# Kernel tuning notes

Hardware: AMD Instinct MI355X
Metric: run time of the kernel (lower is better)

## Reference

```python
import jax, jax.numpy as jnp
import numpy as np

B = 2048      # number of scenes (samples)
A = 64        # max agents per scene
D = 128       # latent_size (embed dim)
H = 4         # heads (hardcoded in module)
HD = D // H   # head dim = 32
NEG = -1e9


def setup_inputs() -> dict:
    key = jax.random.key(0)
    k1, k2, k3, k4 = jax.random.split(key, 4)
    # flat ragged agent features; only the first sum(agents) rows are 'real'
    att_in = jax.random.normal(k1, (B * A, D), dtype=jnp.float32)
    agents_per_sample = jax.random.randint(k2, (B,), 1, A + 1)  # each scene has >=1 agent
    s = 1.0 / np.sqrt(D)
    w_in = jax.random.uniform(k3, (3 * D, D), minval=-s, maxval=s, dtype=jnp.float32)
    b_in = jnp.zeros((3 * D,), dtype=jnp.float32)
    w_out = jax.random.uniform(k4, (D, D), minval=-s, maxval=s, dtype=jnp.float32)
    b_out = jnp.zeros((D,), dtype=jnp.float32)
    return {"att_in": att_in, "w_in": w_in, "b_in": b_in,
            "w_out": w_out, "b_out": b_out, "agents_per_sample": agents_per_sample}


def reference(att_in, w_in, b_in, w_out, b_out, agents_per_sample):
    # scatter flat ragged rows into padded [B, A, D] (same as padded_att_in[mask] = att_in)
    offsets = jnp.cumsum(agents_per_sample) - agents_per_sample          # exclusive prefix sum
    idx = offsets[:, None] + jnp.arange(A)[None, :]                      # [B, A] flat row index
    mask = jnp.arange(A)[None, :] < agents_per_sample[:, None]          # [B, A] valid-agent mask
    padded = jnp.take(att_in, idx, axis=0) * mask[..., None].astype(att_in.dtype)
    # fused in-projection (nn.MultiheadAttention in_proj)
    qkv = padded @ w_in.T + b_in                                        # [B, A, 3D]
    q, k, v = jnp.split(qkv, 3, axis=-1)
    q = q.reshape(B, A, H, HD)
    k = k.reshape(B, A, H, HD)
    v = v.reshape(B, A, H, HD)
    scores = jnp.einsum('bqhd,bkhd->bhqk', q, k) / np.sqrt(HD).astype(q.dtype)
    # key_padding_mask: padded keys excluded from softmax
    scores = jnp.where(mask[:, None, None, :], scores, NEG)
    attn = jax.nn.softmax(scores, axis=-1)
    ctx = jnp.einsum('bhqk,bkhd->bqhd', attn, v).reshape(B, A, D)
    out = (ctx @ w_out.T + b_out) * mask[..., None].astype(ctx.dtype)   # zero out padded rows (torch slices them off)
    return out
```

## Files before the change

### kernel.cpp

```cpp
#include <hip/hip_runtime.h>
#include <hip/hip_bf16.h>

typedef __bf16 bf16;
typedef __bf16 bf16x4 __attribute__((ext_vector_type(4)));
typedef __bf16 bf16x8 __attribute__((ext_vector_type(8)));
typedef float  f32x4  __attribute__((ext_vector_type(4)));

#define NEG_INF (-1e9f)
#define N_SCENES 2048

__global__ __launch_bounds__(256) void prep_kernel(
    const float* __restrict__ w_in, const float* __restrict__ w_out,
    const int* __restrict__ agents,
    bf16* __restrict__ w_in_b, bf16* __restrict__ w_out_b, int* __restrict__ offs)
{
    __shared__ int tot[256];
    const int t = threadIdx.x;
    if (blockIdx.x == 0) {
        int loc[8]; int s = 0;
        #pragma unroll
        for (int j = 0; j < 8; ++j) { loc[j] = agents[t * 8 + j]; s += loc[j]; }
        tot[t] = s;
        __syncthreads();
        for (int o = 1; o < 256; o <<= 1) {
            int v = (t >= o) ? tot[t - o] : 0;
            __syncthreads();
            tot[t] += v;
            __syncthreads();
        }
        int run = tot[t] - s;
        #pragma unroll
        for (int j = 0; j < 8; ++j) { offs[t * 8 + j] = run; run += loc[j]; }
    } else {
        int i = (blockIdx.x - 1) * 1024 + t * 4;
        float4 v; bf16* dst;
        if (i < 49152) { v = *(const float4*)(w_in + i);            dst = w_in_b + i; }
        else           { v = *(const float4*)(w_out + (i - 49152)); dst = w_out_b + (i - 49152); }
        bf16x4 o = { (bf16)v.x, (bf16)v.y, (bf16)v.z, (bf16)v.w };
        *(bf16x4*)dst = o;
    }
}

__global__ __launch_bounds__(256, 3) void attn_kernel(
    const float* __restrict__ att_in,
    const float* __restrict__ b_in, const float* __restrict__ b_out,
    const bf16* __restrict__ w_in_b, const bf16* __restrict__ w_out_b,
    const int* __restrict__ agents, const int* __restrict__ offs,
    float* __restrict__ out)
{
    __shared__ bf16 s_lds[4 * 6144];

    const int b    = blockIdx.x;
    const int tid  = threadIdx.x;
    const int lane = tid & 63;
    const int w    = tid >> 6;
    const int h    = w;
    const int r    = lane & 15;
    const int qd   = lane >> 4;
    const int q1   = qd & 1;
    const int qh   = qd >> 1;
    const int nb   = agents[b];
    const int off  = offs[b];
    const int mtc  = (nb + 15) >> 4;

    bf16* Qld = s_lds + w * 6144;
    bf16* Kld = Qld + 2048;
    bf16* vT  = Qld + 4096;

    {
        const float4 z4 = make_float4(0.f, 0.f, 0.f, 0.f);
        const int nz = (64 - nb) * 32;
        for (int i = tid; i < nz; i += 256) {
            int row = nb + (i >> 5);
            *(float4*)(out + ((size_t)b * 64 + row) * 128 + (i & 31) * 4) = z4;
        }
    }

    {
        bf16x4 z4 = {(bf16)0.f,(bf16)0.f,(bf16)0.f,(bf16)0.f};
        int zrow = lane >> 1, zh = lane & 1;
        #pragma unroll
        for (int u = 2; u < 8; ++u)
            if (u >= 2 * mtc) {
                int uu = u ^ (zrow & 7);
                *(bf16x4*)(vT + zrow * 64 + uu * 8 + zh * 4) = z4;
            }
    }

    bf16x8 xa[4][4];
    #pragma unroll
    for (int mt = 0; mt < 4; ++mt) {
        const int xrow = mt * 16 + r;
        const bool vr = xrow < nb;
        const float* px = att_in + (((size_t)(off + xrow)) << 7) + qd * 8;
        #pragma unroll
        for (int ks = 0; ks < 4; ++ks) {
            float4 lo = make_float4(0.f,0.f,0.f,0.f), hi = lo;
            if (vr) {
                lo = *(const float4*)(px + ks * 32);
                hi = *(const float4*)(px + ks * 32 + 4);
            }
            xa[mt][ks] = (bf16x8){(bf16)lo.x,(bf16)lo.y,(bf16)lo.z,(bf16)lo.w,
                                  (bf16)hi.x,(bf16)hi.y,(bf16)hi.z,(bf16)hi.w};
        }
    }

    #pragma unroll
    for (int t = 0; t < 6; ++t) {
        const int kind = t >> 1, jt = t & 1;
        const int j0 = kind * 128 + h * 32 + jt * 16;
        const bf16* pw = w_in_b + (size_t)(j0 + r) * 128 + qd * 8;
        bf16x8 wb[4];
        #pragma unroll
        for (int ks = 0; ks < 4; ++ks)
            wb[ks] = *(const bf16x8*)(pw + ks * 32);
        if (kind < 2) {
            const float4 b4 = *(const float4*)(b_in + j0 + qd * 4);
            bf16* dst = (kind == 0) ? Qld : Kld;
            #pragma unroll
            for (int mt = 0; mt < 4; ++mt)
                if (mt < mtc) {
                    f32x4 acc = {0.f,0.f,0.f,0.f};
                    #pragma unroll
                    for (int ks = 0; ks < 4; ++ks)
                        acc = __builtin_amdgcn_mfma_f32_16x16x32_bf16(wb[ks], xa[mt][ks], acc, 0, 0, 0);
                    bf16x4 pk = {(bf16)(acc[0]+b4.x), (bf16)(acc[1]+b4.y),
                                 (bf16)(acc[2]+b4.z), (bf16)(acc[3]+b4.w)};
                    int rowa = mt * 16 + r;
                    int uu = (jt * 2 + qh) ^ (rowa & 3);
                    *(bf16x4*)(dst + rowa * 32 + uu * 8 + q1 * 4) = pk;
                }
        } else {
            const float bv = b_in[j0 + r];
            #pragma unroll
            for (int mt = 0; mt < 4; ++mt)
                if (mt < mtc) {
                    f32x4 acc = {0.f,0.f,0.f,0.f};
                    #pragma unroll
                    for (int ks = 0; ks < 4; ++ks)
                        acc = __builtin_amdgcn_mfma_f32_16x16x32_bf16(xa[mt][ks], wb[ks], acc, 0, 0, 0);
                    bf16x4 pk = {(bf16)(acc[0]+bv), (bf16)(acc[1]+bv),
                                 (bf16)(acc[2]+bv), (bf16)(acc[3]+bv)};
                    int rowd = jt * 16 + r;
                    int uu = (mt * 2 + qh) ^ (rowd & 7);
                    *(bf16x4*)(vT + rowd * 64 + uu * 8 + q1 * 4) = pk;
                }
        }
    }

    bf16x8 kf[4];
    #pragma unroll
    for (int nt = 0; nt < 4; ++nt)
        if (nt < mtc) {
            int row = nt * 16 + r;
            kf[nt] = *(const bf16x8*)(Kld + row * 32 + (qd ^ (row & 3)) * 8);
        }
    bf16x8 vf[2][2];
    #pragma unroll
    for (int dt = 0; dt < 2; ++dt)
        #pragma unroll
        for (int hk = 0; hk < 2; ++hk) {
            int row = dt * 16 + r;
            vf[dt][hk] = *(const bf16x8*)(vT + row * 64 + ((hk * 4 + qd) ^ (row & 7)) * 8);
        }
    bf16x8 wof[2][4]; float4 bo4[2];
    #pragma unroll
    for (int t2 = 0; t2 < 2; ++t2) {
        const int jg = (w * 2 + t2) * 16;
        const bf16* pw = w_out_b + (size_t)(jg + r) * 128 + qd * 8;
        #pragma unroll
        for (int s = 0; s < 4; ++s)
            wof[t2][s] = *(const bf16x8*)(pw + s * 32);
        bo4[t2] = *(const float4*)(b_out + jg + qd * 4);
    }

    const float scale = 0.17677669529663687f;

    #pragma unroll
    for (int mt = 0; mt < 4; ++mt)
        if (mt < mtc) {
            int qrow = mt * 16 + r;
            bf16x8 qf = *(const bf16x8*)(Qld + qrow * 32 + (qd ^ (qrow & 3)) * 8);
            f32x4 S[4];
            #pragma unroll
            for (int nt = 0; nt < 4; ++nt)
                if (nt < mtc) {
                    f32x4 z = {0.f,0.f,0.f,0.f};
                    S[nt] = __builtin_amdgcn_mfma_f32_16x16x32_bf16(kf[nt], qf, z, 0, 0, 0);
                }
            float mx = NEG_INF;
            #pragma unroll
            for (int nt = 0; nt < 4; ++nt) {
                if (nt < mtc) {
                    #pragma unroll
                    for (int i = 0; i < 4; ++i) {
                        bool kv = (nt * 16 + qd * 4 + i) < nb;
                        float val = kv ? S[nt][i] * scale : NEG_INF;
                        S[nt][i] = val;
                        mx = fmaxf(mx, val);
                    }
                } else {
                    S[nt] = (f32x4){NEG_INF, NEG_INF, NEG_INF, NEG_INF};
                }
            }
            mx = fmaxf(mx, __shfl_xor(mx, 16));
            mx = fmaxf(mx, __shfl_xor(mx, 32));
            float l = 0.f;
            #pragma unroll
            for (int nt = 0; nt < 4; ++nt)
                #pragma unroll
                for (int i = 0; i < 4; ++i) {
                    float e = __expf(S[nt][i] - mx);
                    S[nt][i] = e; l += e;
                }
            l += __shfl_xor(l, 16);
            l += __shfl_xor(l, 32);
            const float rl = 1.0f / l;
            #pragma unroll
            for (int nt = 0; nt < 4; ++nt)
                #pragma unroll
                for (int i = 0; i < 4; ++i)
                    S[nt][i] *= rl;

            f32x4 o0 = {0.f,0.f,0.f,0.f}, o1 = {0.f,0.f,0.f,0.f};
            #pragma unroll
            for (int hk = 0; hk < 2; ++hk)
                if (hk * 2 < mtc) {
                    float pv[8];
                    #pragma unroll
                    for (int jj = 0; jj < 8; ++jj) {
                        int sl = r + q1 * 32 + (jj >> 2) * 16;
                        float f0 = __shfl(S[2*hk  ][jj & 3], sl);
                        float f1 = __shfl(S[2*hk+1][jj & 3], sl);
                        pv[jj] = (qd < 2) ? f0 : f1;
                    }
                    bf16x8 pf = {(bf16)pv[0],(bf16)pv[1],(bf16)pv[2],(bf16)pv[3],
                                 (bf16)pv[4],(bf16)pv[5],(bf16)pv[6],(bf16)pv[7]};
                    o0 = __builtin_amdgcn_mfma_f32_16x16x32_bf16(vf[0][hk], pf, o0, 0, 0, 0);
                    o1 = __builtin_amdgcn_mfma_f32_16x16x32_bf16(vf[1][hk], pf, o1, 0, 0, 0);
                }

            float cv[8];
            #pragma unroll
            for (int jj = 0; jj < 8; ++jj) {
                int sl = r + q1 * 32 + (jj >> 2) * 16;
                float f0 = __shfl(o0[jj & 3], sl);
                float f1 = __shfl(o1[jj & 3], sl);
                cv[jj] = (qd < 2) ? f0 : f1;
            }
            bf16x8 cf = {(bf16)cv[0],(bf16)cv[1],(bf16)cv[2],(bf16)cv[3],
                         (bf16)cv[4],(bf16)cv[5],(bf16)cv[6],(bf16)cv[7]};
            *(bf16x8*)(Qld + mt * 512 + lane * 8) = cf;
        }
    __syncthreads();

    #pragma unroll
    for (int mt = 0; mt < 4; ++mt)
        if (mt < mtc) {
            bf16x8 cb[4];
            #pragma unroll
            for (int s = 0; s < 4; ++s)
                cb[s] = *(const bf16x8*)(s_lds + s * 6144 + mt * 512 + lane * 8);
            const int rowa = mt * 16 + r;
            #pragma unroll
            for (int t2 = 0; t2 < 2; ++t2) {
                f32x4 acc = {0.f,0.f,0.f,0.f};
                #pragma unroll
                for (int s = 0; s < 4; ++s)
                    acc = __builtin_amdgcn_mfma_f32_16x16x32_bf16(wof[t2][s], cb[s], acc, 0, 0, 0);
                if (rowa < nb) {
                    float4 o4 = make_float4(acc[0] + bo4[t2].x, acc[1] + bo4[t2].y,
                                            acc[2] + bo4[t2].z, acc[3] + bo4[t2].w);
                    *(float4*)(out + ((size_t)b * 64 + rowa) * 128
                               + (w * 2 + t2) * 16 + qd * 4) = o4;
                }
            }
        }
}

extern "C" void kernel_launch(void* const* d_in, const int* in_sizes, int n_in,
                              void* d_out, int out_size, void* d_ws, size_t ws_size,
                              hipStream_t stream)
{
    const float* att_in = (const float*)d_in[0];
    const float* w_in   = (const float*)d_in[1];
    const float* b_in   = (const float*)d_in[2];
    const float* w_out  = (const float*)d_in[3];
    const float* b_out  = (const float*)d_in[4];
    const int*   agents = (const int*)d_in[5];

    bf16* w_in_b  = (bf16*)d_ws;
    bf16* w_out_b = w_in_b + 49152;
    int*  offs    = (int*)((char*)d_ws + 98304 + 32768);

    prep_kernel<<<65, 256, 0, stream>>>(w_in, w_out, agents, w_in_b, w_out_b, offs);
    attn_kernel<<<N_SCENES, 256, 0, stream>>>(att_in, b_in, b_out, w_in_b, w_out_b,
                                              agents, offs, (float*)d_out);
}
```

Baseline: 177.1 us.

## Split each scene's row tiles across two waves per head with 512-thread blocks

Doubles the block to 512 threads so that two waves share each head, each wave handling alternating 16-row tiles. This halves per-wave serial work and register state (xa shrinks from 4x4 to 2x4 fragments). A barrier is added after the QKV projection because K/V written by one wave are now read by its sibling. The w_out fragment loads move into the final projection loop so they no longer stay live across attention. The cost is more barrier synchronisation and redundant per-wave weight loads, with occupancy now set by 512-thread launch bounds.

```diff
diff --git a/kernel.cpp b/kernel.cpp
--- a/kernel.cpp
+++ b/kernel.cpp
@@ -41,7 +41,7 @@
     }
 }
 
-__global__ __launch_bounds__(256, 3) void attn_kernel(
+__global__ __launch_bounds__(512, 6) void attn_kernel(
     const float* __restrict__ att_in,
     const float* __restrict__ b_in, const float* __restrict__ b_out,
     const bf16* __restrict__ w_in_b, const bf16* __restrict__ w_out_b,
@@ -54,7 +54,8 @@
     const int tid  = threadIdx.x;
     const int lane = tid & 63;
     const int w    = tid >> 6;
-    const int h    = w;
+    const int h    = w & 3;
+    const int u    = w >> 2;
     const int r    = lane & 15;
     const int qd   = lane >> 4;
     const int q1   = qd & 1;
@@ -63,33 +64,34 @@
     const int off  = offs[b];
     const int mtc  = (nb + 15) >> 4;
 
-    bf16* Qld = s_lds + w * 6144;
+    bf16* Qld = s_lds + h * 6144;
     bf16* Kld = Qld + 2048;
     bf16* vT  = Qld + 4096;
 
     {
         const float4 z4 = make_float4(0.f, 0.f, 0.f, 0.f);
         const int nz = (64 - nb) * 32;
-        for (int i = tid; i < nz; i += 256) {
+        for (int i = tid; i < nz; i += 512) {
             int row = nb + (i >> 5);
             *(float4*)(out + ((size_t)b * 64 + row) * 128 + (i & 31) * 4) = z4;
         }
     }
 
-    {
+    if (u == 0) {
         bf16x4 z4 = {(bf16)0.f,(bf16)0.f,(bf16)0.f,(bf16)0.f};
         int zrow = lane >> 1, zh = lane & 1;
         #pragma unroll
-        for (int u = 2; u < 8; ++u)
-            if (u >= 2 * mtc) {
-                int uu = u ^ (zrow & 7);
+        for (int un = 2; un < 8; ++un)
+            if (un >= 2 * mtc) {
+                int uu = un ^ (zrow & 7);
                 *(bf16x4*)(vT + zrow * 64 + uu * 8 + zh * 4) = z4;
             }
     }
 
-    bf16x8 xa[4][4];
-    #pragma unroll
-    for (int mt = 0; mt < 4; ++mt) {
+    bf16x8 xa[2][4];
+    #pragma unroll
+    for (int mi = 0; mi < 2; ++mi) {
+        const int mt = u + 2 * mi;
         const int xrow = mt * 16 + r;
         const bool vr = xrow < nb;
         const float* px = att_in + (((size_t)(off + xrow)) << 7) + qd * 8;
@@ -100,7 +102,7 @@
                 lo = *(const float4*)(px + ks * 32);
                 hi = *(const float4*)(px + ks * 32 + 4);
             }
-            xa[mt][ks] = (bf16x8){(bf16)lo.x,(bf16)lo.y,(bf16)lo.z,(bf16)lo.w,
+            xa[mi][ks] = (bf16x8){(bf16)lo.x,(bf16)lo.y,(bf16)lo.z,(bf16)lo.w,
                                   (bf16)hi.x,(bf16)hi.y,(bf16)hi.z,(bf16)hi.w};
         }
     }
@@ -118,35 +120,40 @@
             const float4 b4 = *(const float4*)(b_in + j0 + qd * 4);
             bf16* dst = (kind == 0) ? Qld : Kld;
             #pragma unroll
-            for (int mt = 0; mt < 4; ++mt)
+            for (int mi = 0; mi < 2; ++mi) {
+                const int mt = u + 2 * mi;
                 if (mt < mtc) {
                     f32x4 acc = {0.f,0.f,0.f,0.f};
                     #pragma unroll
                     for (int ks = 0; ks < 4; ++ks)
-                        acc = __builtin_amdgcn_mfma_f32_16x16x32_bf16(wb[ks], xa[mt][ks], acc, 0, 0, 0);
+                        acc = __builtin_amdgcn_mfma_f32_16x16x32_bf16(wb[ks], xa[mi][ks], acc, 0, 0, 0);
                     bf16x4 pk = {(bf16)(acc[0]+b4.x), (bf16)(acc[1]+b4.y),
                                  (bf16)(acc[2]+b4.z), (bf16)(acc[3]+b4.w)};
                     int rowa = mt * 16 + r;
                     int uu = (jt * 2 + qh) ^ (rowa & 3);
                     *(bf16x4*)(dst + rowa * 32 + uu * 8 + q1 * 4) = pk;
                 }
+            }
         } else {
             const float bv = b_in[j0 + r];
             #pragma unroll
-            for (int mt = 0; mt < 4; ++mt)
+            for (int mi = 0; mi < 2; ++mi) {
+                const int mt = u + 2 * mi;
                 if (mt < mtc) {
                     f32x4 acc = {0.f,0.f,0.f,0.f};
                     #pragma unroll
                     for (int ks = 0; ks < 4; ++ks)
-                        acc = __builtin_amdgcn_mfma_f32_16x16x32_bf16(xa[mt][ks], wb[ks], acc, 0, 0, 0);
+                        acc = __builtin_amdgcn_mfma_f32_16x16x32_bf16(xa[mi][ks], wb[ks], acc, 0, 0, 0);
                     bf16x4 pk = {(bf16)(acc[0]+bv), (bf16)(acc[1]+bv),
                                  (bf16)(acc[2]+bv), (bf16)(acc[3]+bv)};
                     int rowd = jt * 16 + r;
                     int uu = (mt * 2 + qh) ^ (rowd & 7);
                     *(bf16x4*)(vT + rowd * 64 + uu * 8 + q1 * 4) = pk;
                 }
-        }
-    }
+            }
+        }
+    }
+    __syncthreads();
 
     bf16x8 kf[4];
     #pragma unroll
@@ -163,21 +170,12 @@
             int row = dt * 16 + r;
             vf[dt][hk] = *(const bf16x8*)(vT + row * 64 + ((hk * 4 + qd) ^ (row & 7)) * 8);
         }
-    bf16x8 wof[2][4]; float4 bo4[2];
-    #pragma unroll
-    for (int t2 = 0; t2 < 2; ++t2) {
-        const int jg = (w * 2 + t2) * 16;
-        const bf16* pw = w_out_b + (size_t)(jg + r) * 128 + qd * 8;
-        #pragma unroll
-        for (int s = 0; s < 4; ++s)
-            wof[t2][s] = *(const bf16x8*)(pw + s * 32);
-        bo4[t2] = *(const float4*)(b_out + jg + qd * 4);
-    }
 
     const float scale = 0.17677669529663687f;
 
     #pragma unroll
-    for (int mt = 0; mt < 4; ++mt)
+    for (int mi = 0; mi < 2; ++mi) {
+        const int mt = u + 2 * mi;
         if (mt < mtc) {
             int qrow = mt * 16 + r;
             bf16x8 qf = *(const bf16x8*)(Qld + qrow * 32 + (qd ^ (qrow & 3)) * 8);
@@ -252,30 +250,39 @@
                          (bf16)cv[4],(bf16)cv[5],(bf16)cv[6],(bf16)cv[7]};
             *(bf16x8*)(Qld + mt * 512 + lane * 8) = cf;
         }
+    }
     __syncthreads();
 
     #pragma unroll
-    for (int mt = 0; mt < 4; ++mt)
-        if (mt < mtc) {
-            bf16x8 cb[4];
-            #pragma unroll
-            for (int s = 0; s < 4; ++s)
-                cb[s] = *(const bf16x8*)(s_lds + s * 6144 + mt * 512 + lane * 8);
-            const int rowa = mt * 16 + r;
-            #pragma unroll
-            for (int t2 = 0; t2 < 2; ++t2) {
+    for (int t2 = 0; t2 < 2; ++t2) {
+        const int jg = (h * 2 + t2) * 16;
+        const bf16* pw = w_out_b + (size_t)(jg + r) * 128 + qd * 8;
+        bf16x8 wof[4];
+        #pragma unroll
+        for (int s = 0; s < 4; ++s)
+            wof[s] = *(const bf16x8*)(pw + s * 32);
+        const float4 bo4 = *(const float4*)(b_out + jg + qd * 4);
+        #pragma unroll
+        for (int mi = 0; mi < 2; ++mi) {
+            const int mt = u + 2 * mi;
+            if (mt < mtc) {
+                bf16x8 cb[4];
+                #pragma unroll
+                for (int s = 0; s < 4; ++s)
+                    cb[s] = *(const bf16x8*)(s_lds + s * 6144 + mt * 512 + lane * 8);
                 f32x4 acc = {0.f,0.f,0.f,0.f};
                 #pragma unroll
                 for (int s = 0; s < 4; ++s)
-                    acc = __builtin_amdgcn_mfma_f32_16x16x32_bf16(wof[t2][s], cb[s], acc, 0, 0, 0);
+                    acc = __builtin_amdgcn_mfma_f32_16x16x32_bf16(wof[s], cb[s], acc, 0, 0, 0);
+                const int rowa = mt * 16 + r;
                 if (rowa < nb) {
-                    float4 o4 = make_float4(acc[0] + bo4[t2].x, acc[1] + bo4[t2].y,
-                                            acc[2] + bo4[t2].z, acc[3] + bo4[t2].w);
-                    *(float4*)(out + ((size_t)b * 64 + rowa) * 128
-                               + (w * 2 + t2) * 16 + qd * 4) = o4;
-                }
-            }
-        }
+                    float4 o4 = make_float4(acc[0] + bo4.x, acc[1] + bo4.y,
+                                            acc[2] + bo4.z, acc[3] + bo4.w);
+                    *(float4*)(out + ((size_t)b * 64 + rowa) * 128 + jg + qd * 4) = o4;
+                }
+            }
+        }
+    }
 }
 
 extern "C" void kernel_launch(void* const* d_in, const int* in_sizes, int n_in,
@@ -294,6 +301,6 @@
     int*  offs    = (int*)((char*)d_ws + 98304 + 32768);
 
     prep_kernel<<<65, 256, 0, stream>>>(w_in, w_out, agents, w_in_b, w_out_b, offs);
-    attn_kernel<<<N_SCENES, 256, 0, stream>>>(att_in, b_in, b_out, w_in_b, w_out_b,
+    attn_kernel<<<N_SCENES, 512, 0, stream>>>(att_in, b_in, b_out, w_in_b, w_out_b,
                                               agents, offs, (float*)d_out);
 }
```

Result: slower. 217.5 us (+22.8%).

## Keep Q in registers, transpose fragments via permlane32 swap, cut LDS footprint

Applied to the files above, without the earlier changes.

Q projection results stay in registers and are transposed into the MFMA operand layout with v_permlane32_swap plus xor-shuffles, so the per-wave Q tile in LDS goes away. LDS per block shrinks from 48KB to 32KB and launch bounds rise to 4 blocks per CU. The P and context re-layouts now pack to bf16 pairs before shuffling instead of doing 16 float shuffles, and softmax uses exp2 with a log2e-folded scale and tree reductions. Holding Q in registers adds register pressure under the tighter occupancy target, and the permlane builtin requires gfx950 support.

```diff
diff --git a/kernel.cpp b/kernel.cpp
--- a/kernel.cpp
+++ b/kernel.cpp
@@ -2,12 +2,54 @@
 #include <hip/hip_bf16.h>
 
 typedef __bf16 bf16;
+typedef __bf16 bf16x2 __attribute__((ext_vector_type(2)));
 typedef __bf16 bf16x4 __attribute__((ext_vector_type(4)));
 typedef __bf16 bf16x8 __attribute__((ext_vector_type(8)));
 typedef float  f32x4  __attribute__((ext_vector_type(4)));
+typedef int    i32x2  __attribute__((ext_vector_type(2)));
+typedef int    i32x4  __attribute__((ext_vector_type(4)));
 
 #define NEG_INF (-1e9f)
 #define N_SCENES 2048
+
+#if defined(__has_builtin)
+#if __has_builtin(__builtin_amdgcn_exp2f)
+#define EXP2(x) __builtin_amdgcn_exp2f(x)
+#endif
+#endif
+#ifndef EXP2
+#define EXP2(x) exp2f(x)
+#endif
+
+static __device__ __forceinline__ void pl32(int& a, int& b) {
+#if defined(__has_builtin) && __has_builtin(__builtin_amdgcn_permlane32_swap)
+    i32x2 res = __builtin_amdgcn_permlane32_swap(a, b, false, false);
+    a = res[0]; b = res[1];
+#else
+    asm("v_permlane32_swap_b32 %0, %1" : "+v"(a), "+v"(b));
+#endif
+}
+
+static __device__ __forceinline__ int pk2(float x, float y) {
+    bf16x2 t = {(bf16)x, (bf16)y};
+    return __builtin_bit_cast(int, t);
+}
+
+static __device__ __forceinline__ i32x4 qtrans(int a0, int a1, int b0, int b1,
+                                               bool qodd) {
+    i32x4 out;
+    pl32(a0, b0);
+    int y2 = __shfl_xor(b0, 16);
+    int x2 = __shfl_xor(a0, 16);
+    out[0] = qodd ? y2 : a0;
+    out[2] = qodd ? b0 : x2;
+    pl32(a1, b1);
+    int y2b = __shfl_xor(b1, 16);
+    int x2b = __shfl_xor(a1, 16);
+    out[1] = qodd ? y2b : a1;
+    out[3] = qodd ? b1 : x2b;
+    return out;
+}
 
 __global__ __launch_bounds__(256) void prep_kernel(
     const float* __restrict__ w_in, const float* __restrict__ w_out,
@@ -41,14 +83,14 @@
     }
 }
 
-__global__ __launch_bounds__(256, 3) void attn_kernel(
+__global__ __launch_bounds__(256, 4) void attn_kernel(
     const float* __restrict__ att_in,
     const float* __restrict__ b_in, const float* __restrict__ b_out,
     const bf16* __restrict__ w_in_b, const bf16* __restrict__ w_out_b,
     const int* __restrict__ agents, const int* __restrict__ offs,
     float* __restrict__ out)
 {
-    __shared__ bf16 s_lds[4 * 6144];
+    __shared__ bf16 s_lds[4 * 4096];
 
     const int b    = blockIdx.x;
     const int tid  = threadIdx.x;
@@ -59,13 +101,13 @@
     const int qd   = lane >> 4;
     const int q1   = qd & 1;
     const int qh   = qd >> 1;
+    const bool qodd = (q1 != 0);
     const int nb   = agents[b];
     const int off  = offs[b];
     const int mtc  = (nb + 15) >> 4;
 
-    bf16* Qld = s_lds + w * 6144;
-    bf16* Kld = Qld + 2048;
-    bf16* vT  = Qld + 4096;
+    bf16* Kld = s_lds + h * 4096;
+    bf16* vT  = Kld + 2048;
 
     {
         const float4 z4 = make_float4(0.f, 0.f, 0.f, 0.f);
@@ -80,9 +122,9 @@
         bf16x4 z4 = {(bf16)0.f,(bf16)0.f,(bf16)0.f,(bf16)0.f};
         int zrow = lane >> 1, zh = lane & 1;
         #pragma unroll
-        for (int u = 2; u < 8; ++u)
-            if (u >= 2 * mtc) {
-                int uu = u ^ (zrow & 7);
+        for (int un = 2; un < 8; ++un)
+            if (un >= 2 * mtc) {
+                int uu = un ^ (zrow & 7);
                 *(bf16x4*)(vT + zrow * 64 + uu * 8 + zh * 4) = z4;
             }
     }
@@ -105,47 +147,74 @@
         }
     }
 
-    #pragma unroll
-    for (int t = 0; t < 6; ++t) {
-        const int kind = t >> 1, jt = t & 1;
-        const int j0 = kind * 128 + h * 32 + jt * 16;
+    bf16x4 qreg[4][2];
+    #pragma unroll
+    for (int jt = 0; jt < 2; ++jt) {
+        const int j0 = h * 32 + jt * 16;
         const bf16* pw = w_in_b + (size_t)(j0 + r) * 128 + qd * 8;
         bf16x8 wb[4];
         #pragma unroll
         for (int ks = 0; ks < 4; ++ks)
             wb[ks] = *(const bf16x8*)(pw + ks * 32);
-        if (kind < 2) {
-            const float4 b4 = *(const float4*)(b_in + j0 + qd * 4);
-            bf16* dst = (kind == 0) ? Qld : Kld;
-            #pragma unroll
-            for (int mt = 0; mt < 4; ++mt)
-                if (mt < mtc) {
-                    f32x4 acc = {0.f,0.f,0.f,0.f};
-                    #pragma unroll
-                    for (int ks = 0; ks < 4; ++ks)
-                        acc = __builtin_amdgcn_mfma_f32_16x16x32_bf16(wb[ks], xa[mt][ks], acc, 0, 0, 0);
-                    bf16x4 pk = {(bf16)(acc[0]+b4.x), (bf16)(acc[1]+b4.y),
-                                 (bf16)(acc[2]+b4.z), (bf16)(acc[3]+b4.w)};
-                    int rowa = mt * 16 + r;
-                    int uu = (jt * 2 + qh) ^ (rowa & 3);
-                    *(bf16x4*)(dst + rowa * 32 + uu * 8 + q1 * 4) = pk;
-                }
-        } else {
-            const float bv = b_in[j0 + r];
-            #pragma unroll
-            for (int mt = 0; mt < 4; ++mt)
-                if (mt < mtc) {
-                    f32x4 acc = {0.f,0.f,0.f,0.f};
-                    #pragma unroll
-                    for (int ks = 0; ks < 4; ++ks)
-                        acc = __builtin_amdgcn_mfma_f32_16x16x32_bf16(xa[mt][ks], wb[ks], acc, 0, 0, 0);
-                    bf16x4 pk = {(bf16)(acc[0]+bv), (bf16)(acc[1]+bv),
-                                 (bf16)(acc[2]+bv), (bf16)(acc[3]+bv)};
-                    int rowd = jt * 16 + r;
-                    int uu = (mt * 2 + qh) ^ (rowd & 7);
-                    *(bf16x4*)(vT + rowd * 64 + uu * 8 + q1 * 4) = pk;
-                }
-        }
+        const float4 b4 = *(const float4*)(b_in + j0 + qd * 4);
+        #pragma unroll
+        for (int mt = 0; mt < 4; ++mt)
+            if (mt < mtc) {
+                f32x4 acc = {0.f,0.f,0.f,0.f};
+                #pragma unroll
+                for (int ks = 0; ks < 4; ++ks)
+                    acc = __builtin_amdgcn_mfma_f32_16x16x32_bf16(wb[ks], xa[mt][ks], acc, 0, 0, 0);
+                qreg[mt][jt] = (bf16x4){(bf16)(acc[0]+b4.x), (bf16)(acc[1]+b4.y),
+                                        (bf16)(acc[2]+b4.z), (bf16)(acc[3]+b4.w)};
+            }
+    }
+
+    #pragma unroll
+    for (int jt = 0; jt < 2; ++jt) {
+        const int j0 = 128 + h * 32 + jt * 16;
+        const bf16* pw = w_in_b + (size_t)(j0 + r) * 128 + qd * 8;
+        bf16x8 wb[4];
+        #pragma unroll
+        for (int ks = 0; ks < 4; ++ks)
+            wb[ks] = *(const bf16x8*)(pw + ks * 32);
+        const float4 b4 = *(const float4*)(b_in + j0 + qd * 4);
+        #pragma unroll
+        for (int mt = 0; mt < 4; ++mt)
+            if (mt < mtc) {
+                f32x4 acc = {0.f,0.f,0.f,0.f};
+                #pragma unroll
+                for (int ks = 0; ks < 4; ++ks)
+                    acc = __builtin_amdgcn_mfma_f32_16x16x32_bf16(wb[ks], xa[mt][ks], acc, 0, 0, 0);
+                bf16x4 pk = {(bf16)(acc[0]+b4.x), (bf16)(acc[1]+b4.y),
+                             (bf16)(acc[2]+b4.z), (bf16)(acc[3]+b4.w)};
+                int rowa = mt * 16 + r;
+                int uu = (jt * 2 + qh) ^ (rowa & 3);
+                *(bf16x4*)(Kld + rowa * 32 + uu * 8 + q1 * 4) = pk;
+            }
+    }
+
+    #pragma unroll
+    for (int jt = 0; jt < 2; ++jt) {
+        const int j0 = 256 + h * 32 + jt * 16;
+        const bf16* pw = w_in_b + (size_t)(j0 + r) * 128 + qd * 8;
+        bf16x8 wb[4];
+        #pragma unroll
+        for (int ks = 0; ks < 4; ++ks)
+            wb[ks] = *(const bf16x8*)(pw + ks * 32);
+        const float bv = b_in[j0 + r];
+        #pragma unroll
+        for (int mt = 0; mt < 4; ++mt)
+            if (mt < mtc) {
+                f32x4 acc = {0.f,0.f,0.f,0.f};
+                #pragma unroll
+                for (int ks = 0; ks < 4; ++ks)
+                    acc = __builtin_amdgcn_mfma_f32_16x16x32_bf16(xa[mt][ks], wb[ks], acc, 0, 0, 0);
+                bf16x4 pk = {(bf16)(acc[0]+bv), (bf16)(acc[1]+bv),
+                             (bf16)(acc[2]+bv), (bf16)(acc[3]+bv)};
+                int rowd = jt * 16 + r;
+                int uu = (mt * 2 + qh) ^ (rowd & 7);
+                *(bf16x4*)(vT + rowd * 64 + uu * 8 + q1 * 4) = pk;
+            }
     }
 
     bf16x8 kf[4];
@@ -166,7 +235,7 @@
     bf16x8 wof[2][4]; float4 bo4[2];
     #pragma unroll
     for (int t2 = 0; t2 < 2; ++t2) {
-        const int jg = (w * 2 + t2) * 16;
+        const int jg = (h * 2 + t2) * 16;
         const bf16* pw = w_out_b + (size_t)(jg + r) * 128 + qd * 8;
         #pragma unroll
         for (int s = 0; s < 4; ++s)
@@ -174,13 +243,16 @@
         bo4[t2] = *(const float4*)(b_out + jg + qd * 4);
     }
 
-    const float scale = 0.17677669529663687f;
+    const float k1 = 0.25503484f;
 
     #pragma unroll
     for (int mt = 0; mt < 4; ++mt)
         if (mt < mtc) {
-            int qrow = mt * 16 + r;
-            bf16x8 qf = *(const bf16x8*)(Qld + qrow * 32 + (qd ^ (qrow & 3)) * 8);
+            i32x2 qa = __builtin_bit_cast(i32x2, qreg[mt][0]);
+            i32x2 qb = __builtin_bit_cast(i32x2, qreg[mt][1]);
+            i32x4 qw = qtrans(qa[0], qa[1], qb[0], qb[1], qodd);
+            bf16x8 qf = __builtin_bit_cast(bf16x8, qw);
+
             f32x4 S[4];
             #pragma unroll
             for (int nt = 0; nt < 4; ++nt)
@@ -188,31 +260,34 @@
                     f32x4 z = {0.f,0.f,0.f,0.f};
                     S[nt] = __builtin_amdgcn_mfma_f32_16x16x32_bf16(kf[nt], qf, z, 0, 0, 0);
                 }
-            float mx = NEG_INF;
             #pragma unroll
             for (int nt = 0; nt < 4; ++nt) {
                 if (nt < mtc) {
                     #pragma unroll
                     for (int i = 0; i < 4; ++i) {
                         bool kv = (nt * 16 + qd * 4 + i) < nb;
-                        float val = kv ? S[nt][i] * scale : NEG_INF;
-                        S[nt][i] = val;
-                        mx = fmaxf(mx, val);
+                        S[nt][i] = kv ? S[nt][i] * k1 : NEG_INF;
                     }
                 } else {
                     S[nt] = (f32x4){NEG_INF, NEG_INF, NEG_INF, NEG_INF};
                 }
             }
+            float tm[4];
+            #pragma unroll
+            for (int nt = 0; nt < 4; ++nt)
+                tm[nt] = fmaxf(fmaxf(S[nt][0], S[nt][1]), fmaxf(S[nt][2], S[nt][3]));
+            float mx = fmaxf(fmaxf(tm[0], tm[1]), fmaxf(tm[2], tm[3]));
             mx = fmaxf(mx, __shfl_xor(mx, 16));
             mx = fmaxf(mx, __shfl_xor(mx, 32));
-            float l = 0.f;
-            #pragma unroll
-            for (int nt = 0; nt < 4; ++nt)
-                #pragma unroll
-                for (int i = 0; i < 4; ++i) {
-                    float e = __expf(S[nt][i] - mx);
-                    S[nt][i] = e; l += e;
-                }
+            float lt[4];
+            #pragma unroll
+            for (int nt = 0; nt < 4; ++nt) {
+                float e0 = EXP2(S[nt][0] - mx), e1 = EXP2(S[nt][1] - mx);
+                float e2 = EXP2(S[nt][2] - mx), e3 = EXP2(S[nt][3] - mx);
+                S[nt][0] = e0; S[nt][1] = e1; S[nt][2] = e2; S[nt][3] = e3;
+                lt[nt] = (e0 + e1) + (e2 + e3);
+            }
+            float l = (lt[0] + lt[1]) + (lt[2] + lt[3]);
             l += __shfl_xor(l, 16);
             l += __shfl_xor(l, 32);
             const float rl = 1.0f / l;
@@ -226,31 +301,25 @@
             #pragma unroll
             for (int hk = 0; hk < 2; ++hk)
                 if (hk * 2 < mtc) {
-                    float pv[8];
-                    #pragma unroll
-                    for (int jj = 0; jj < 8; ++jj) {
-                        int sl = r + q1 * 32 + (jj >> 2) * 16;
-                        float f0 = __shfl(S[2*hk  ][jj & 3], sl);
-                        float f1 = __shfl(S[2*hk+1][jj & 3], sl);
-                        pv[jj] = (qd < 2) ? f0 : f1;
-                    }
-                    bf16x8 pf = {(bf16)pv[0],(bf16)pv[1],(bf16)pv[2],(bf16)pv[3],
-                                 (bf16)pv[4],(bf16)pv[5],(bf16)pv[6],(bf16)pv[7]};
+                    int a0 = pk2(S[2*hk  ][0], S[2*hk  ][1]);
+                    int a1 = pk2(S[2*hk  ][2], S[2*hk  ][3]);
+                    int b0 = pk2(S[2*hk+1][0], S[2*hk+1][1]);
+                    int b1 = pk2(S[2*hk+1][2], S[2*hk+1][3]);
+                    i32x4 pw4 = qtrans(a0, a1, b0, b1, qodd);
+                    bf16x8 pf = __builtin_bit_cast(bf16x8, pw4);
                     o0 = __builtin_amdgcn_mfma_f32_16x16x32_bf16(vf[0][hk], pf, o0, 0, 0, 0);
                     o1 = __builtin_amdgcn_mfma_f32_16x16x32_bf16(vf[1][hk], pf, o1, 0, 0, 0);
                 }
 
-            float cv[8];
-            #pragma unroll
-            for (int jj = 0; jj < 8; ++jj) {
-                int sl = r + q1 * 32 + (jj >> 2) * 16;
-                float f0 = __shfl(o0[jj & 3], sl);
-                float f1 = __shfl(o1[jj & 3], sl);
-                cv[jj] = (qd < 2) ? f0 : f1;
-            }
-            bf16x8 cf = {(bf16)cv[0],(bf16)cv[1],(bf16)cv[2],(bf16)cv[3],
-                         (bf16)cv[4],(bf16)cv[5],(bf16)cv[6],(bf16)cv[7]};
-            *(bf16x8*)(Qld + mt * 512 + lane * 8) = cf;
+            {
+                int a0 = pk2(o0[0], o0[1]);
+                int a1 = pk2(o0[2], o0[3]);
+                int b0 = pk2(o1[0], o1[1]);
+                int b1 = pk2(o1[2], o1[3]);
+                i32x4 cw = qtrans(a0, a1, b0, b1, qodd);
+                bf16x8 cf = __builtin_bit_cast(bf16x8, cw);
+                *(bf16x8*)(Kld + mt * 512 + lane * 8) = cf;
+            }
         }
     __syncthreads();
 
@@ -260,7 +329,7 @@
             bf16x8 cb[4];
             #pragma unroll
             for (int s = 0; s < 4; ++s)
-                cb[s] = *(const bf16x8*)(s_lds + s * 6144 + mt * 512 + lane * 8);
+                cb[s] = *(const bf16x8*)(s_lds + s * 4096 + mt * 512 + lane * 8);
             const int rowa = mt * 16 + r;
             #pragma unroll
             for (int t2 = 0; t2 < 2; ++t2) {
```

Result: faster. 170.6 us (median of 2 runs) (-3.7%).
